# Kernel tuning notes

Hardware: AMD Instinct MI355X
Metric: run time of the kernel (lower is better)

## Reference

```python
import math
import jax, jax.numpy as jnp
import numpy as np

B, S, D_MODEL, H = 2, 2048, 1024, 16
D_HEAD = D_MODEL // H
NEG = -90000000000.0


def setup_inputs() -> dict:
    key = jax.random.key(0)
    ks = jax.random.split(key, 12)
    scale = 1.0 / math.sqrt(D_MODEL)
    return {
        "Q": jax.random.normal(ks[0], (B, S, D_MODEL), jnp.float32),
        "K": jax.random.normal(ks[1], (B, S, D_MODEL), jnp.float32),
        "V": jax.random.normal(ks[2], (B, S, D_MODEL), jnp.float32),
        "mask": jax.random.randint(ks[3], (B, 1, S, S), 0, 2).astype(bool),
        "Wq": jax.random.normal(ks[4], (D_MODEL, D_MODEL), jnp.float32) * scale,
        "bq": jnp.zeros((D_MODEL,), jnp.float32),
        "Wk": jax.random.normal(ks[5], (D_MODEL, D_MODEL), jnp.float32) * scale,
        "bk": jnp.zeros((D_MODEL,), jnp.float32),
        "Wv": jax.random.normal(ks[6], (D_MODEL, D_MODEL), jnp.float32) * scale,
        "bv": jnp.zeros((D_MODEL,), jnp.float32),
        "Wo": jax.random.normal(ks[7], (D_MODEL, D_MODEL), jnp.float32) * scale,
        "bo": jnp.zeros((D_MODEL,), jnp.float32),
    }


def _split_heads(x):
    # (B, S, D) -> (B, H, S, Dh)
    b, s, _ = x.shape
    return x.reshape(b, s, H, D_HEAD).transpose(0, 2, 1, 3)


def reference(Q, K, V, mask, Wq, bq, Wk, bk, Wv, bv, Wo, bo):
    q = _split_heads(Q @ Wq.T + bq)
    k = _split_heads(K @ Wk.T + bk)
    v = _split_heads(V @ Wv.T + bv)
    # scaled dot product with additive mask (mask.float() * -9e10)
    scores = jnp.einsum("bhqd,bhkd->bhqk", q, k) / math.sqrt(D_HEAD)
    scores = scores + mask.astype(scores.dtype) * NEG
    attn = jax.nn.softmax(scores, axis=-1)
    ctx = jnp.einsum("bhqk,bhkd->bhqd", attn, v)  # (B, H, S, Dh)
    ctx = ctx.transpose(0, 2, 1, 3).reshape(Q.shape[0], q.shape[2], D_MODEL)
    return ctx @ Wo.T + bo
```

## Files before the change

### kernel.cpp

```cpp
#include <hip/hip_runtime.h>
#include <hip/hip_bf16.h>


typedef __bf16 bf16x8 __attribute__((ext_vector_type(8)));
typedef __bf16 bf16x4 __attribute__((ext_vector_type(4)));
typedef float f32x4 __attribute__((ext_vector_type(4)));

#define S_LEN 2048
#define DM 1024
#define NH 16
#define DH 64
#define MROWS 4096

#define QSCALE 0.18033688011112042f

static __device__ __forceinline__ unsigned short f2bf(float f) {
    __bf16 b = (__bf16)f;
    unsigned short u; __builtin_memcpy(&u, &b, 2); return u;
}

static __device__ __forceinline__ float exp2_hw(float x) {
#if __has_builtin(__builtin_amdgcn_exp2f)
    return __builtin_amdgcn_exp2f(x);
#else
    float r; asm("v_exp_f32 %0, %1" : "=v"(r) : "v"(x)); return r;
#endif
}

static __device__ __forceinline__ bf16x8 cvt8(float4 a, float4 b) {
    bf16x8 o;
    o[0] = (__bf16)a.x; o[1] = (__bf16)a.y; o[2] = (__bf16)a.z; o[3] = (__bf16)a.w;
    o[4] = (__bf16)b.x; o[5] = (__bf16)b.y; o[6] = (__bf16)b.z; o[7] = (__bf16)b.w;
    return o;
}

__global__ __launch_bounds__(256)
void prep(const int* __restrict__ m, unsigned* __restrict__ mb,
          const float* __restrict__ Q, unsigned short* __restrict__ dQ,
          const float* __restrict__ K, unsigned short* __restrict__ dK,
          const float* __restrict__ V, unsigned short* __restrict__ dV,
          const float* __restrict__ W0, unsigned short* __restrict__ dW0,
          const float* __restrict__ W1, unsigned short* __restrict__ dW1,
          const float* __restrict__ W2, unsigned short* __restrict__ dW2,
          const float* __restrict__ W3, unsigned short* __restrict__ dW3)
{
    const int bx = blockIdx.x, tid = threadIdx.x;
    if (bx < 1024) {
        const int lane = tid & 63, w = tid >> 6;
        const int row = bx * 4 + w;
        const int* src = m + (size_t)row * S_LEN;
        unsigned* dst = mb + (size_t)row * (S_LEN / 32);
        for (int i = 0; i < 32; i++) {
            int v = src[i * 64 + lane];
            unsigned long long bm = __ballot(v != 0);
            if (lane == 0) { dst[i*2] = (unsigned)bm; dst[i*2+1] = (unsigned)(bm >> 32); }
        }
    } else if (bx < 7168) {
        int t = bx - 1024;
        int which = t >> 11;
        const float* s = which == 0 ? Q : which == 1 ? K : V;
        unsigned short* d = which == 0 ? dQ : which == 1 ? dK : dV;
        int i = ((t & 2047) * 256 + tid) * 8;
        float4 a = *(const float4*)(s + i);
        float4 b = *(const float4*)(s + i + 4);
        *(bf16x8*)(d + i) = cvt8(a, b);
    } else {
        int t = bx - 7168;
        int which = t >> 9;
        const float* s = which == 0 ? W0 : which == 1 ? W1 : which == 2 ? W2 : W3;
        unsigned short* d = which == 0 ? dW0 : which == 1 ? dW1 : which == 2 ? dW2 : dW3;
        int i = ((t & 511) * 256 + tid) * 8;
        float4 a = *(const float4*)(s + i);
        float4 b = *(const float4*)(s + i + 4);
        *(bf16x8*)(d + i) = cvt8(a, b);
    }
}

__global__ __launch_bounds__(256)
void gemm128(const unsigned short* __restrict__ X0, const unsigned short* __restrict__ X1,
             const unsigned short* __restrict__ X2,
             const unsigned short* __restrict__ W0, const unsigned short* __restrict__ W1,
             const unsigned short* __restrict__ W2,
             const float* __restrict__ b0, const float* __restrict__ b1,
             const float* __restrict__ b2,
             unsigned short* __restrict__ d0, unsigned short* __restrict__ d1,
             unsigned short* __restrict__ d2)
{
    __shared__ __align__(16) unsigned short As[128 * 32];
    __shared__ __align__(16) unsigned short Bs[128 * 32];

    const int bid = blockIdx.x + blockIdx.y * 8 + blockIdx.z * 256;
    const int xcd = bid & 7;
    const int t   = bid >> 3;
    const int z   = t >> 5;
    const int u   = t & 31;
    const int nt  = u & 7;
    const int mt  = xcd * 4 + (u >> 3);

    const unsigned short* X = z == 0 ? X0 : z == 1 ? X1 : X2;
    const unsigned short* W = z == 0 ? W0 : z == 1 ? W1 : W2;
    const float* bias        = z == 0 ? b0 : z == 1 ? b1 : b2;
    unsigned short* dstb     = z == 0 ? d0 : z == 1 ? d1 : d2;

    const int tid  = threadIdx.x;
    const int m0   = mt * 128;
    const int n0   = nt * 128;
    const int lane = tid & 63;
    const int w    = tid >> 6;
    const int wm   = (w >> 1) * 64, wn = (w & 1) * 64;
    const int lr   = lane & 15;
    const int lg   = lane >> 4;

    f32x4 acc[4][4];
#pragma unroll
    for (int i = 0; i < 4; i++)
#pragma unroll
        for (int j = 0; j < 4; j++) acc[i][j] = f32x4{0.f, 0.f, 0.f, 0.f};

    for (int k0 = 0; k0 < DM; k0 += 32) {
        __syncthreads();
#pragma unroll
        for (int j = 0; j < 2; j++) {
            int e = tid + j * 256;
            int row = e >> 2, c8 = (e & 3) * 8;
            __builtin_amdgcn_global_load_lds(
                (const __attribute__((address_space(1))) unsigned*)&X[(size_t)(m0 + row) * DM + k0 + c8],
                (__attribute__((address_space(3))) unsigned*)&As[e * 8], 16, 0, 0);
            __builtin_amdgcn_global_load_lds(
                (const __attribute__((address_space(1))) unsigned*)&W[(size_t)(n0 + row) * DM + k0 + c8],
                (__attribute__((address_space(3))) unsigned*)&Bs[e * 8], 16, 0, 0);
        }
        __syncthreads();
        bf16x8 af[4], bfr[4];
#pragma unroll
        for (int mi = 0; mi < 4; mi++)
            af[mi] = *(const bf16x8*)(&As[(wm + mi * 16 + lr) * 32 + lg * 8]);
#pragma unroll
        for (int ni = 0; ni < 4; ni++)
            bfr[ni] = *(const bf16x8*)(&Bs[(wn + ni * 16 + lr) * 32 + lg * 8]);
#pragma unroll
        for (int mi = 0; mi < 4; mi++)
#pragma unroll
            for (int ni = 0; ni < 4; ni++)
                acc[mi][ni] = __builtin_amdgcn_mfma_f32_16x16x32_bf16(
                    af[mi], bfr[ni], acc[mi][ni], 0, 0, 0);
    }

#pragma unroll
    for (int mi = 0; mi < 4; mi++) {
#pragma unroll
        for (int ni = 0; ni < 4; ni++) {
            const int gcol = n0 + wn + ni * 16 + lr;
            const float bv = bias[gcol];
            const int grow0 = m0 + wm + mi * 16 + lg * 4;
            if (z == 2) {
                int b = grow0 >> 11, s = grow0 & (S_LEN - 1);
                int h = gcol >> 6, dh = gcol & 63;
                bf16x4 pk;
#pragma unroll
                for (int r = 0; r < 4; r++) pk[r] = (__bf16)(acc[mi][ni][r] + bv);
                size_t di = ((size_t)(b * NH + h) * DH + dh) * S_LEN + s;
                *(bf16x4*)(&dstb[di]) = pk;
            } else {
#pragma unroll
                for (int r = 0; r < 4; r++) {
                    int grow = grow0 + r;
                    float v = acc[mi][ni][r] + bv;
                    if (z == 0) v *= QSCALE;
                    int b = grow >> 11, s = grow & (S_LEN - 1);
                    int h = gcol >> 6, dh = gcol & 63;
                    dstb[((size_t)(b * NH + h) * S_LEN + s) * DH + dh] = f2bf(v);
                }
            }
        }
    }
}

__global__ __launch_bounds__(256, 4)
void gemm_out(const unsigned short* __restrict__ X, const unsigned short* __restrict__ W,
              const float* __restrict__ bias, float* __restrict__ dst)
{
    __shared__ __align__(16) unsigned short As[128 * 32];
    __shared__ __align__(16) unsigned short Bs[64 * 32];

    const int bid = blockIdx.x + blockIdx.y * 16;
    const int xcd = bid & 7;
    const int u   = bid >> 3;
    const int nt  = u & 15;
    const int mt  = xcd * 4 + (u >> 4);

    const int tid  = threadIdx.x;
    const int m0   = mt * 128;
    const int n0   = nt * 64;
    const int lane = tid & 63;
    const int w    = tid >> 6;
    const int wm   = (w >> 1) * 64, wn = (w & 1) * 32;
    const int lr   = lane & 15;
    const int lg   = lane >> 4;

    f32x4 acc[4][2];
#pragma unroll
    for (int i = 0; i < 4; i++)
#pragma unroll
        for (int j = 0; j < 2; j++) acc[i][j] = f32x4{0.f, 0.f, 0.f, 0.f};

    for (int k0 = 0; k0 < DM; k0 += 32) {
        __syncthreads();
#pragma unroll
        for (int j = 0; j < 2; j++) {
            int e = tid + j * 256;
            int row = e >> 2, c8 = (e & 3) * 8;
            __builtin_amdgcn_global_load_lds(
                (const __attribute__((address_space(1))) unsigned*)&X[(size_t)(m0 + row) * DM + k0 + c8],
                (__attribute__((address_space(3))) unsigned*)&As[e * 8], 16, 0, 0);
        }
        {
            int row = tid >> 2, c8 = (tid & 3) * 8;
            __builtin_amdgcn_global_load_lds(
                (const __attribute__((address_space(1))) unsigned*)&W[(size_t)(n0 + row) * DM + k0 + c8],
                (__attribute__((address_space(3))) unsigned*)&Bs[tid * 8], 16, 0, 0);
        }
        __syncthreads();
        bf16x8 af[4], bfr[2];
#pragma unroll
        for (int mi = 0; mi < 4; mi++)
            af[mi] = *(const bf16x8*)(&As[(wm + mi * 16 + lr) * 32 + lg * 8]);
#pragma unroll
        for (int ni = 0; ni < 2; ni++)
            bfr[ni] = *(const bf16x8*)(&Bs[(wn + ni * 16 + lr) * 32 + lg * 8]);
#pragma unroll
        for (int mi = 0; mi < 4; mi++)
#pragma unroll
            for (int ni = 0; ni < 2; ni++)
                acc[mi][ni] = __builtin_amdgcn_mfma_f32_16x16x32_bf16(
                    af[mi], bfr[ni], acc[mi][ni], 0, 0, 0);
    }
#pragma unroll
    for (int mi = 0; mi < 4; mi++)
#pragma unroll
        for (int ni = 0; ni < 2; ni++) {
            const int gcol = n0 + wn + ni * 16 + lr;
            const float bv = bias[gcol];
            const int grow0 = m0 + wm + mi * 16 + lg * 4;
#pragma unroll
            for (int r = 0; r < 4; r++)
                dst[(size_t)(grow0 + r) * DM + gcol] = acc[mi][ni][r] + bv;
        }
}

__global__ __launch_bounds__(256, 3)
void attn(const unsigned short* __restrict__ q_ws,
          const unsigned short* __restrict__ k_ws,
          const unsigned short* __restrict__ vt_ws,
          const unsigned* __restrict__ mbits,
          unsigned short* __restrict__ ctx)
{
    __shared__ __align__(16) unsigned short Ks[2][64 * 72];
    __shared__ __align__(16) unsigned short Vs[2][64 * 72];
    __shared__ __align__(16) unsigned short Pq[4][16 * 72];
    const int tid = threadIdx.x, lane = tid & 63, w = tid >> 6;
    const int lr = lane & 15, lg = lane >> 4;

    const int i    = blockIdx.x;
    const int xcd  = i & 7;
    const int slot = i >> 3;
    const int bh   = xcd * 4 + (slot >> 4);
    const int qblk = slot & 15;
    const int b  = bh >> 4;
    const int h  = bh & 15;
    const int q0 = qblk * 128 + w * 32;
    const int qA = q0 + lr;
    const int qB = q0 + 16 + lr;

    const int srow = tid >> 3;
    const int sseg = tid & 7;

    const unsigned short* qh = q_ws + (size_t)bh * S_LEN * DH;
    const unsigned short* kh = k_ws + (size_t)bh * S_LEN * DH;
    const unsigned short* vh = vt_ws + (size_t)bh * DH * S_LEN;
    const unsigned* mrA = mbits + (size_t)(b * S_LEN + qA) * (S_LEN / 32);
    const unsigned* mrB = mbits + (size_t)(b * S_LEN + qB) * (S_LEN / 32);

    bf16x8 aqA[2], aqB[2];
#pragma unroll
    for (int c = 0; c < 2; c++) {
        aqA[c] = *(const bf16x8*)(&qh[(size_t)qA * DH + c * 32 + lg * 8]);
        aqB[c] = *(const bf16x8*)(&qh[(size_t)qB * DH + c * 32 + lg * 8]);
    }

    bf16x8 ones;
#pragma unroll
    for (int j = 0; j < 8; j++) ones[j] = (__bf16)1.0f;

    f32x4 accA[4], accB[4], accRA, accRB;
#pragma unroll
    for (int di = 0; di < 4; di++) {
        accA[di] = f32x4{0.f, 0.f, 0.f, 0.f};
        accB[di] = f32x4{0.f, 0.f, 0.f, 0.f};
    }
    accRA = f32x4{0.f, 0.f, 0.f, 0.f};
    accRB = f32x4{0.f, 0.f, 0.f, 0.f};

    uint4 kreg0, kreg1, vreg0, vreg1;
    kreg0 = *(const uint4*)(&kh[(size_t)(srow)      * DH + sseg * 8]);
    kreg1 = *(const uint4*)(&kh[(size_t)(srow + 32) * DH + sseg * 8]);
    vreg0 = *(const uint4*)(&vh[(size_t)(srow)      * S_LEN + sseg * 8]);
    vreg1 = *(const uint4*)(&vh[(size_t)(srow + 32) * S_LEN + sseg * 8]);
    *(uint4*)(&Ks[0][(srow)      * 72 + sseg * 8]) = kreg0;
    *(uint4*)(&Ks[0][(srow + 32) * 72 + sseg * 8]) = kreg1;
    *(uint4*)(&Vs[0][(srow)      * 72 + sseg * 8]) = vreg0;
    *(uint4*)(&Vs[0][(srow + 32) * 72 + sseg * 8]) = vreg1;
    kreg0 = *(const uint4*)(&kh[(size_t)(64 + srow)      * DH + sseg * 8]);
    kreg1 = *(const uint4*)(&kh[(size_t)(64 + srow + 32) * DH + sseg * 8]);
    vreg0 = *(const uint4*)(&vh[(size_t)(srow)      * S_LEN + 64 + sseg * 8]);
    vreg1 = *(const uint4*)(&vh[(size_t)(srow + 32) * S_LEN + 64 + sseg * 8]);
    __syncthreads();

    unsigned short* pq = &Pq[w][0];

    for (int it = 0; it < 32; it++) {
        const int cur = it & 1;
        const unsigned short* Kc = &Ks[cur][0];
        const unsigned short* Vc = &Vs[cur][0];
        if (it < 31) {
            unsigned short* Kn = &Ks[cur ^ 1][0];
            unsigned short* Vn = &Vs[cur ^ 1][0];
            *(uint4*)(&Kn[(srow)      * 72 + sseg * 8]) = kreg0;
            *(uint4*)(&Kn[(srow + 32) * 72 + sseg * 8]) = kreg1;
            *(uint4*)(&Vn[(srow)      * 72 + sseg * 8]) = vreg0;
            *(uint4*)(&Vn[(srow + 32) * 72 + sseg * 8]) = vreg1;
        }
        if (it < 30) {
            const int kn = (it + 2) * 64;
            kreg0 = *(const uint4*)(&kh[(size_t)(kn + srow)      * DH + sseg * 8]);
            kreg1 = *(const uint4*)(&kh[(size_t)(kn + srow + 32) * DH + sseg * 8]);
            vreg0 = *(const uint4*)(&vh[(size_t)(srow)      * S_LEN + kn + sseg * 8]);
            vreg1 = *(const uint4*)(&vh[(size_t)(srow + 32) * S_LEN + kn + sseg * 8]);
        }

        const uint2 mwA = *(const uint2*)(&mrA[it * 2]);
        const uint2 mwB = *(const uint2*)(&mrB[it * 2]);

        f32x4 sA[4], sB[4];
#pragma unroll
        for (int ni = 0; ni < 4; ni++) {
            bf16x8 ak0 = *(const bf16x8*)(&Kc[(ni * 16 + lr) * 72 + lg * 8]);
            bf16x8 ak1 = *(const bf16x8*)(&Kc[(ni * 16 + lr) * 72 + 32 + lg * 8]);
            f32x4 tA = __builtin_amdgcn_mfma_f32_16x16x32_bf16(ak0, aqA[0], f32x4{0.f,0.f,0.f,0.f}, 0,0,0);
            tA = __builtin_amdgcn_mfma_f32_16x16x32_bf16(ak1, aqA[1], tA, 0,0,0);
            f32x4 tB = __builtin_amdgcn_mfma_f32_16x16x32_bf16(ak0, aqB[0], f32x4{0.f,0.f,0.f,0.f}, 0,0,0);
            tB = __builtin_amdgcn_mfma_f32_16x16x32_bf16(ak1, aqB[1], tB, 0,0,0);
            sA[ni] = tA; sB[ni] = tB;
        }

#pragma unroll
        for (int ni = 0; ni < 4; ni++) {
            unsigned wA = (ni & 2) ? mwA.y : mwA.x;
            unsigned wB = (ni & 2) ? mwB.y : mwB.x;
            unsigned nibA = wA >> ((ni & 1) * 16 + lg * 4);
            unsigned nibB = wB >> ((ni & 1) * 16 + lg * 4);
#pragma unroll
            for (int r = 0; r < 4; r++) {
                float pA = exp2_hw(sA[ni][r]);
                float pB = exp2_hw(sB[ni][r]);
                sA[ni][r] = (nibA & (1u << r)) ? 0.f : pA;
                sB[ni][r] = (nibB & (1u << r)) ? 0.f : pB;
            }
        }

        bf16x8 av0[4], av1[4];
#pragma unroll
        for (int ni = 0; ni < 4; ni++) {
            bf16x4 pkA;
#pragma unroll
            for (int r = 0; r < 4; r++) pkA[r] = (__bf16)sA[ni][r];
            *(bf16x4*)(&pq[lr * 72 + ni * 16 + lg * 4]) = pkA;
        }
        bf16x8 bpA0 = *(const bf16x8*)(&pq[lr * 72 + lg * 8]);
        bf16x8 bpA1 = *(const bf16x8*)(&pq[lr * 72 + 32 + lg * 8]);
#pragma unroll
        for (int di = 0; di < 4; di++) {
            av0[di] = *(const bf16x8*)(&Vc[(di * 16 + lr) * 72 + lg * 8]);
            av1[di] = *(const bf16x8*)(&Vc[(di * 16 + lr) * 72 + 32 + lg * 8]);
            accA[di] = __builtin_amdgcn_mfma_f32_16x16x32_bf16(av0[di], bpA0, accA[di], 0, 0, 0);
            accA[di] = __builtin_amdgcn_mfma_f32_16x16x32_bf16(av1[di], bpA1, accA[di], 0, 0, 0);
        }
        accRA = __builtin_amdgcn_mfma_f32_16x16x32_bf16(ones, bpA0, accRA, 0, 0, 0);
        accRA = __builtin_amdgcn_mfma_f32_16x16x32_bf16(ones, bpA1, accRA, 0, 0, 0);

#pragma unroll
        for (int ni = 0; ni < 4; ni++) {
            bf16x4 pkB;
#pragma unroll
            for (int r = 0; r < 4; r++) pkB[r] = (__bf16)sB[ni][r];
            *(bf16x4*)(&pq[lr * 72 + ni * 16 + lg * 4]) = pkB;
        }
        bf16x8 bpB0 = *(const bf16x8*)(&pq[lr * 72 + lg * 8]);
        bf16x8 bpB1 = *(const bf16x8*)(&pq[lr * 72 + 32 + lg * 8]);
#pragma unroll
        for (int di = 0; di < 4; di++) {
            accB[di] = __builtin_amdgcn_mfma_f32_16x16x32_bf16(av0[di], bpB0, accB[di], 0, 0, 0);
            accB[di] = __builtin_amdgcn_mfma_f32_16x16x32_bf16(av1[di], bpB1, accB[di], 0, 0, 0);
        }
        accRB = __builtin_amdgcn_mfma_f32_16x16x32_bf16(ones, bpB0, accRB, 0, 0, 0);
        accRB = __builtin_amdgcn_mfma_f32_16x16x32_bf16(ones, bpB1, accRB, 0, 0, 0);

        __syncthreads();
    }

    const float invA = 1.0f / fmaxf(accRA[0], 1e-37f);
    const float invB = 1.0f / fmaxf(accRB[0], 1e-37f);

    unsigned short* crowA = &ctx[((size_t)(b * S_LEN + qA)) * DM + h * DH];
    unsigned short* crowB = &ctx[((size_t)(b * S_LEN + qB)) * DM + h * DH];
#pragma unroll
    for (int di = 0; di < 4; di++) {
        bf16x4 oA, oB;
#pragma unroll
        for (int r = 0; r < 4; r++) {
            oA[r] = (__bf16)(accA[di][r] * invA);
            oB[r] = (__bf16)(accB[di][r] * invB);
        }
        *(bf16x4*)(&crowA[di * 16 + lg * 4]) = oA;
        *(bf16x4*)(&crowB[di * 16 + lg * 4]) = oB;
    }
}

extern "C" void kernel_launch(void* const* d_in, const int* in_sizes, int n_in,
                              void* d_out, int out_size, void* d_ws, size_t ws_size,
                              hipStream_t stream)
{
    (void)in_sizes; (void)n_in; (void)out_size; (void)ws_size;
    const float* Q  = (const float*)d_in[0];
    const float* K  = (const float*)d_in[1];
    const float* V  = (const float*)d_in[2];
    const int*   Mk = (const int*)d_in[3];
    const float* Wq = (const float*)d_in[4];
    const float* bq = (const float*)d_in[5];
    const float* Wk = (const float*)d_in[6];
    const float* bk = (const float*)d_in[7];
    const float* Wv = (const float*)d_in[8];
    const float* bv = (const float*)d_in[9];
    const float* Wo = (const float*)d_in[10];
    const float* bo = (const float*)d_in[11];

    const int NX = MROWS * DM;
    const int NW = DM * DM;

    unsigned short* q_ws  = (unsigned short*)d_ws;
    unsigned short* k_ws  = q_ws + (size_t)NX;
    unsigned short* vt_ws = k_ws + (size_t)NX;
    unsigned short* ctx   = vt_ws + (size_t)NX;
    unsigned*       mbits = (unsigned*)(ctx + (size_t)NX);
    unsigned short* Wbq   = (unsigned short*)(mbits + (size_t)MROWS * (S_LEN / 32));
    unsigned short* Wbk   = Wbq + (size_t)NW;
    unsigned short* Wbv   = Wbk + (size_t)NW;
    unsigned short* Wbo   = Wbv + (size_t)NW;
    unsigned short* Xbq   = Wbo + (size_t)NW;
    unsigned short* Xbk   = Xbq + (size_t)NX;
    unsigned short* Xbv   = Xbk + (size_t)NX;
    float* out = (float*)d_out;

    dim3 blk(256);
    prep<<<dim3(9216), blk, 0, stream>>>(Mk, mbits, Q, Xbq, K, Xbk, V, Xbv,
                                         Wq, Wbq, Wk, Wbk, Wv, Wbv, Wo, Wbo);

    gemm128<<<dim3(8, 32, 3), blk, 0, stream>>>(Xbq, Xbk, Xbv, Wbq, Wbk, Wbv,
                                                bq, bk, bv, q_ws, k_ws, vt_ws);

    attn<<<dim3(512), blk, 0, stream>>>(q_ws, k_ws, vt_ws, mbits, ctx);

    gemm_out<<<dim3(16, 32), blk, 0, stream>>>(ctx, Wbo, bo, out);
}
```

Baseline: 265.0 us.

## Drop LDS staging in attention; load K/V straight to registers, permlane P transpose

After: 335.5 us. +26.6%, slower.

```diff
diff --git a/kernel.cpp b/kernel.cpp
--- a/kernel.cpp
+++ b/kernel.cpp
@@ -25,6 +25,18 @@
 #else
     float r; asm("v_exp_f32 %0, %1" : "=v"(r) : "v"(x)); return r;
 #endif
+}
+
+static __device__ __forceinline__ unsigned cvtpk_bf16(float lo, float hi) {
+    unsigned r;
+    asm("v_cvt_pk_bf16_f32 %0, %1, %2" : "=v"(r) : "v"(lo), "v"(hi));
+    return r;
+}
+static __device__ __forceinline__ void pl32swap(unsigned &x, unsigned &y) {
+    asm volatile("v_permlane32_swap_b32 %0, %1" : "+v"(x), "+v"(y));
+}
+static __device__ __forceinline__ void pl16swap(unsigned &x, unsigned &y) {
+    asm volatile("v_permlane16_swap_b32 %0, %1" : "+v"(x), "+v"(y));
 }
 
 static __device__ __forceinline__ bf16x8 cvt8(float4 a, float4 b) {
@@ -248,16 +260,13 @@
         }
 }
 
-__global__ __launch_bounds__(256, 3)
+__global__ __launch_bounds__(256, 2)
 void attn(const unsigned short* __restrict__ q_ws,
           const unsigned short* __restrict__ k_ws,
           const unsigned short* __restrict__ vt_ws,
           const unsigned* __restrict__ mbits,
           unsigned short* __restrict__ ctx)
 {
-    __shared__ __align__(16) unsigned short Ks[2][64 * 72];
-    __shared__ __align__(16) unsigned short Vs[2][64 * 72];
-    __shared__ __align__(16) unsigned short Pq[4][16 * 72];
     const int tid = threadIdx.x, lane = tid & 63, w = tid >> 6;
     const int lr = lane & 15, lg = lane >> 4;
 
@@ -272,9 +281,6 @@
     const int qA = q0 + lr;
     const int qB = q0 + 16 + lr;
 
-    const int srow = tid >> 3;
-    const int sseg = tid & 7;
-
     const unsigned short* qh = q_ws + (size_t)bh * S_LEN * DH;
     const unsigned short* kh = k_ws + (size_t)bh * S_LEN * DH;
     const unsigned short* vh = vt_ws + (size_t)bh * DH * S_LEN;
@@ -301,57 +307,39 @@
     accRA = f32x4{0.f, 0.f, 0.f, 0.f};
     accRB = f32x4{0.f, 0.f, 0.f, 0.f};
 
-    uint4 kreg0, kreg1, vreg0, vreg1;
-    kreg0 = *(const uint4*)(&kh[(size_t)(srow)      * DH + sseg * 8]);
-    kreg1 = *(const uint4*)(&kh[(size_t)(srow + 32) * DH + sseg * 8]);
-    vreg0 = *(const uint4*)(&vh[(size_t)(srow)      * S_LEN + sseg * 8]);
-    vreg1 = *(const uint4*)(&vh[(size_t)(srow + 32) * S_LEN + sseg * 8]);
-    *(uint4*)(&Ks[0][(srow)      * 72 + sseg * 8]) = kreg0;
-    *(uint4*)(&Ks[0][(srow + 32) * 72 + sseg * 8]) = kreg1;
-    *(uint4*)(&Vs[0][(srow)      * 72 + sseg * 8]) = vreg0;
-    *(uint4*)(&Vs[0][(srow + 32) * 72 + sseg * 8]) = vreg1;
-    kreg0 = *(const uint4*)(&kh[(size_t)(64 + srow)      * DH + sseg * 8]);
-    kreg1 = *(const uint4*)(&kh[(size_t)(64 + srow + 32) * DH + sseg * 8]);
-    vreg0 = *(const uint4*)(&vh[(size_t)(srow)      * S_LEN + 64 + sseg * 8]);
-    vreg1 = *(const uint4*)(&vh[(size_t)(srow + 32) * S_LEN + 64 + sseg * 8]);
-    __syncthreads();
-
-    unsigned short* pq = &Pq[w][0];
-
     for (int it = 0; it < 32; it++) {
-        const int cur = it & 1;
-        const unsigned short* Kc = &Ks[cur][0];
-        const unsigned short* Vc = &Vs[cur][0];
-        if (it < 31) {
-            unsigned short* Kn = &Ks[cur ^ 1][0];
-            unsigned short* Vn = &Vs[cur ^ 1][0];
-            *(uint4*)(&Kn[(srow)      * 72 + sseg * 8]) = kreg0;
-            *(uint4*)(&Kn[(srow + 32) * 72 + sseg * 8]) = kreg1;
-            *(uint4*)(&Vn[(srow)      * 72 + sseg * 8]) = vreg0;
-            *(uint4*)(&Vn[(srow + 32) * 72 + sseg * 8]) = vreg1;
-        }
-        if (it < 30) {
-            const int kn = (it + 2) * 64;
-            kreg0 = *(const uint4*)(&kh[(size_t)(kn + srow)      * DH + sseg * 8]);
-            kreg1 = *(const uint4*)(&kh[(size_t)(kn + srow + 32) * DH + sseg * 8]);
-            vreg0 = *(const uint4*)(&vh[(size_t)(srow)      * S_LEN + kn + sseg * 8]);
-            vreg1 = *(const uint4*)(&vh[(size_t)(srow + 32) * S_LEN + kn + sseg * 8]);
-        }
+        const int kv0 = it * 64;
+
+        bf16x8 av[4][2];
+#pragma unroll
+        for (int di = 0; di < 4; di++)
+#pragma unroll
+            for (int c = 0; c < 2; c++)
+                av[di][c] = *(const bf16x8*)(
+                    &vh[(size_t)(di * 16 + lr) * S_LEN + kv0 + c * 32 + lg * 8]);
 
         const uint2 mwA = *(const uint2*)(&mrA[it * 2]);
         const uint2 mwB = *(const uint2*)(&mrB[it * 2]);
 
         f32x4 sA[4], sB[4];
+        bf16x8 ak[4][2];
+#pragma unroll
+        for (int ni = 0; ni < 4; ni++)
+#pragma unroll
+            for (int c = 0; c < 2; c++)
+                ak[ni][c] = *(const bf16x8*)(
+                    &kh[(size_t)(kv0 + ni * 16 + lr) * DH + c * 32 + lg * 8]);
+
+        __builtin_amdgcn_s_setprio(1);
 #pragma unroll
         for (int ni = 0; ni < 4; ni++) {
-            bf16x8 ak0 = *(const bf16x8*)(&Kc[(ni * 16 + lr) * 72 + lg * 8]);
-            bf16x8 ak1 = *(const bf16x8*)(&Kc[(ni * 16 + lr) * 72 + 32 + lg * 8]);
-            f32x4 tA = __builtin_amdgcn_mfma_f32_16x16x32_bf16(ak0, aqA[0], f32x4{0.f,0.f,0.f,0.f}, 0,0,0);
-            tA = __builtin_amdgcn_mfma_f32_16x16x32_bf16(ak1, aqA[1], tA, 0,0,0);
-            f32x4 tB = __builtin_amdgcn_mfma_f32_16x16x32_bf16(ak0, aqB[0], f32x4{0.f,0.f,0.f,0.f}, 0,0,0);
-            tB = __builtin_amdgcn_mfma_f32_16x16x32_bf16(ak1, aqB[1], tB, 0,0,0);
+            f32x4 tA = __builtin_amdgcn_mfma_f32_16x16x32_bf16(ak[ni][0], aqA[0], f32x4{0.f,0.f,0.f,0.f}, 0,0,0);
+            tA = __builtin_amdgcn_mfma_f32_16x16x32_bf16(ak[ni][1], aqA[1], tA, 0,0,0);
+            f32x4 tB = __builtin_amdgcn_mfma_f32_16x16x32_bf16(ak[ni][0], aqB[0], f32x4{0.f,0.f,0.f,0.f}, 0,0,0);
+            tB = __builtin_amdgcn_mfma_f32_16x16x32_bf16(ak[ni][1], aqB[1], tB, 0,0,0);
             sA[ni] = tA; sB[ni] = tB;
         }
+        __builtin_amdgcn_s_setprio(0);
 
 #pragma unroll
         for (int ni = 0; ni < 4; ni++) {
@@ -368,44 +356,44 @@
             }
         }
 
-        bf16x8 av0[4], av1[4];
+        unsigned wpA[8], wpB[8];
 #pragma unroll
         for (int ni = 0; ni < 4; ni++) {
-            bf16x4 pkA;
-#pragma unroll
-            for (int r = 0; r < 4; r++) pkA[r] = (__bf16)sA[ni][r];
-            *(bf16x4*)(&pq[lr * 72 + ni * 16 + lg * 4]) = pkA;
-        }
-        bf16x8 bpA0 = *(const bf16x8*)(&pq[lr * 72 + lg * 8]);
-        bf16x8 bpA1 = *(const bf16x8*)(&pq[lr * 72 + 32 + lg * 8]);
+            wpA[ni*2]   = cvtpk_bf16(sA[ni][0], sA[ni][1]);
+            wpA[ni*2+1] = cvtpk_bf16(sA[ni][2], sA[ni][3]);
+            wpB[ni*2]   = cvtpk_bf16(sB[ni][0], sB[ni][1]);
+            wpB[ni*2+1] = cvtpk_bf16(sB[ni][2], sB[ni][3]);
+        }
+#pragma unroll
+        for (int c = 0; c < 2; c++) {
+            pl32swap(wpA[c*4 + 0], wpA[c*4 + 2]);
+            pl32swap(wpA[c*4 + 1], wpA[c*4 + 3]);
+            pl16swap(wpA[c*4 + 0], wpA[c*4 + 2]);
+            pl16swap(wpA[c*4 + 1], wpA[c*4 + 3]);
+            pl32swap(wpB[c*4 + 0], wpB[c*4 + 2]);
+            pl32swap(wpB[c*4 + 1], wpB[c*4 + 3]);
+            pl16swap(wpB[c*4 + 0], wpB[c*4 + 2]);
+            pl16swap(wpB[c*4 + 1], wpB[c*4 + 3]);
+        }
+        bf16x8 bpA0, bpA1, bpB0, bpB1;
+        __builtin_memcpy(&bpA0, &wpA[0], 16);
+        __builtin_memcpy(&bpA1, &wpA[4], 16);
+        __builtin_memcpy(&bpB0, &wpB[0], 16);
+        __builtin_memcpy(&bpB1, &wpB[4], 16);
+
+        __builtin_amdgcn_s_setprio(1);
 #pragma unroll
         for (int di = 0; di < 4; di++) {
-            av0[di] = *(const bf16x8*)(&Vc[(di * 16 + lr) * 72 + lg * 8]);
-            av1[di] = *(const bf16x8*)(&Vc[(di * 16 + lr) * 72 + 32 + lg * 8]);
-            accA[di] = __builtin_amdgcn_mfma_f32_16x16x32_bf16(av0[di], bpA0, accA[di], 0, 0, 0);
-            accA[di] = __builtin_amdgcn_mfma_f32_16x16x32_bf16(av1[di], bpA1, accA[di], 0, 0, 0);
+            accA[di] = __builtin_amdgcn_mfma_f32_16x16x32_bf16(av[di][0], bpA0, accA[di], 0, 0, 0);
+            accA[di] = __builtin_amdgcn_mfma_f32_16x16x32_bf16(av[di][1], bpA1, accA[di], 0, 0, 0);
+            accB[di] = __builtin_amdgcn_mfma_f32_16x16x32_bf16(av[di][0], bpB0, accB[di], 0, 0, 0);
+            accB[di] = __builtin_amdgcn_mfma_f32_16x16x32_bf16(av[di][1], bpB1, accB[di], 0, 0, 0);
         }
         accRA = __builtin_amdgcn_mfma_f32_16x16x32_bf16(ones, bpA0, accRA, 0, 0, 0);
         accRA = __builtin_amdgcn_mfma_f32_16x16x32_bf16(ones, bpA1, accRA, 0, 0, 0);
-
-#pragma unroll
-        for (int ni = 0; ni < 4; ni++) {
-            bf16x4 pkB;
-#pragma unroll
-            for (int r = 0; r < 4; r++) pkB[r] = (__bf16)sB[ni][r];
-            *(bf16x4*)(&pq[lr * 72 + ni * 16 + lg * 4]) = pkB;
-        }
-        bf16x8 bpB0 = *(const bf16x8*)(&pq[lr * 72 + lg * 8]);
-        bf16x8 bpB1 = *(const bf16x8*)(&pq[lr * 72 + 32 + lg * 8]);
-#pragma unroll
-        for (int di = 0; di < 4; di++) {
-            accB[di] = __builtin_amdgcn_mfma_f32_16x16x32_bf16(av0[di], bpB0, accB[di], 0, 0, 0);
-            accB[di] = __builtin_amdgcn_mfma_f32_16x16x32_bf16(av1[di], bpB1, accB[di], 0, 0, 0);
-        }
         accRB = __builtin_amdgcn_mfma_f32_16x16x32_bf16(ones, bpB0, accRB, 0, 0, 0);
         accRB = __builtin_amdgcn_mfma_f32_16x16x32_bf16(ones, bpB1, accRB, 0, 0, 0);
-
-        __syncthreads();
+        __builtin_amdgcn_s_setprio(0);
     }
 
     const float invA = 1.0f / fmaxf(accRA[0], 1e-37f);
```
